# Performance work log

Hardware: AMD Instinct MI355X
Metric: run time of the kernel (lower is better)

The kernel has to match this reference:

```python
import jax, jax.numpy as jnp
import numpy as np

VOCAB, EMBED, UNITS, T, B = 50000, 300, 512, 128, 512


def setup_inputs() -> dict:
    key = jax.random.key(0)
    k1, k2, k3, k4 = jax.random.split(key, 4)
    input_sequence = jax.random.randint(k1, (B, T), 0, VOCAB, dtype=jnp.int32)
    state_h = jnp.zeros((B, UNITS), jnp.float32)
    state_c = jnp.zeros((B, UNITS), jnp.float32)
    # learned params (Keras LSTMCell gate order: i, f, g(cell), o)
    emb_table = jax.random.normal(k2, (VOCAB, EMBED), jnp.float32) * 0.05
    kernel = jax.random.normal(k3, (EMBED, 4 * UNITS), jnp.float32) * 0.05
    rec_kernel = jax.random.normal(k4, (UNITS, 4 * UNITS), jnp.float32) * 0.05
    bias = jnp.zeros((4 * UNITS,), jnp.float32)
    return {"input_sequence": input_sequence, "state_h": state_h, "state_c": state_c,
            "emb_table": emb_table, "kernel": kernel, "rec_kernel": rec_kernel, "bias": bias}


def reference(input_sequence, state_h, state_c, emb_table, kernel, rec_kernel, bias):
    # Embedding with mask_zero=True: token id 0 is masked (state carried through).
    x = emb_table[input_sequence]            # [B, T, E]
    mask = (input_sequence != 0)             # [B, T]
    x_t = jnp.transpose(x, (1, 0, 2))        # [T, B, E]
    m_t = jnp.transpose(mask, (1, 0))        # [T, B]

    def step(carry, inp):
        h, c = carry
        xt, mt = inp
        z = xt @ kernel + h @ rec_kernel + bias          # [B, 4U]
        i, f, g, o = jnp.split(z, 4, axis=-1)
        i = jax.nn.sigmoid(i)
        f = jax.nn.sigmoid(f)
        o = jax.nn.sigmoid(o)
        c_new = f * c + i * jnp.tanh(g)
        h_new = o * jnp.tanh(c_new)
        m = mt[:, None]
        h_new = jnp.where(m, h_new, h)
        c_new = jnp.where(m, c_new, c)
        return (h_new, c_new), h_new

    (h_fin, c_fin), outs = jax.lax.scan(step, (state_h, state_c), (x_t, m_t))
    enc_output = jnp.transpose(outs, (1, 0, 2))          # [B, T, U]
    return enc_output, h_fin, c_fin
```

## Files before the change

kernel.cpp:

```cpp
#include <hip/hip_runtime.h>

#define BATCH 512
#define SEQ   128
#define EMBED 300
#define UNITS 512

typedef short  short8   __attribute__((ext_vector_type(8)));
typedef float  floatx16 __attribute__((ext_vector_type(16)));

#define KXF  19
#define KHF  32

#define SH_B1  0
#define SH_B2  32768
#define SMEM_BYTES (32768 + 38912)

#define WS_FLAGS 0
#define WS_HBUF  4096
#define WS_XBUF  (4096 + 1048576)
#define WS_NEED  (WS_XBUF + 2 * 8 * 38912)

__device__ __forceinline__ unsigned short f2bf(float f) {
  union { float f; unsigned u; } v; v.f = f;
  unsigned r = v.u + 0x7fff + ((v.u >> 16) & 1);
  return (unsigned short)(r >> 16);
}
__device__ __forceinline__ float sigm(float x) { return 1.f / (1.f + __expf(-x)); }
__device__ __forceinline__ float tanh_f(float x) {
  float e = __expf(2.f * x);
  return 1.f - 2.f / (e + 1.f);
}

__device__ __forceinline__ void g_store32(unsigned* p, unsigned v) {
  __hip_atomic_store(p, v, __ATOMIC_RELAXED, __HIP_MEMORY_SCOPE_AGENT);
}
__device__ __forceinline__ unsigned long long g_load64(const void* p) {
  return __hip_atomic_load((const unsigned long long*)p, __ATOMIC_RELAXED,
                           __HIP_MEMORY_SCOPE_AGENT);
}
__device__ __forceinline__ short8 ld_frag(const char* p) {
  union { unsigned long long q[2]; short8 s; } u;
  u.q[0] = g_load64(p);
  u.q[1] = g_load64(p + 8);
  return u.s;
}

__device__ __forceinline__ void poll_ge(const unsigned* gf, int lane, unsigned tgt) {
  const unsigned* p = gf + (lane & 31) * 4;
  for (;;) {
    unsigned v = __hip_atomic_load(p, __ATOMIC_RELAXED, __HIP_MEMORY_SCOPE_AGENT);
    if (__ballot(v >= tgt) == ~0ull) break;
    __builtin_amdgcn_s_sleep(1);
  }
}

#define LDH_GRP(arr, base)                                         \
  do { _Pragma("unroll")                                           \
    for (int j = 0; j < 8; ++j) arr[j] = ld_frag(hrow + ((base) + j) * 32); \
  } while (0)

#define MFMA_H_GRP(arr, base)                                                     \
  do { _Pragma("unroll")                                                          \
    for (int j = 0; j < 8; ++j) {                                                 \
      const int kf = (base) + j;                                                  \
      acc0 = __builtin_amdgcn_mfma_f32_32x32x16_bf16(arr[j], b0[kf], acc0, 0,0,0);\
      short8 p1 = *(const short8*)(sh_b1 + (kf * 64 + lane) * 16);                \
      acc1 = __builtin_amdgcn_mfma_f32_32x32x16_bf16(arr[j], p1, acc1, 0,0,0);    \
    }                                                                             \
  } while (0)

extern "C" __global__ void __launch_bounds__(128, 1)
lstm_enc(const int* __restrict__ seq, const float* __restrict__ h0,
         const float* __restrict__ c0, const float* __restrict__ emb,
         const float* __restrict__ kern, const float* __restrict__ rkern,
         const float* __restrict__ bias, float* __restrict__ out,
         char* __restrict__ ws)
{
  extern __shared__ __align__(16) char smem[];
  char* sh_b1 = smem + SH_B1;
  char* sh_b2 = smem + SH_B2;

  const int tid  = threadIdx.x;
  const int lane = tid & 63;
  const int w    = tid >> 6;
  const int rb   = blockIdx.x & 7;
  const int ug   = blockIdx.x >> 3;

  unsigned* gflags = (unsigned*)(ws + WS_FLAGS) + rb * 128;
  unsigned* myflag = gflags + ug * 4;
  char* hb_[2] = { ws + WS_HBUF, ws + WS_HBUF + 524288 };
  char* xb_[2] = { ws + WS_XBUF + (0 * 8 + rb) * 38912,
                   ws + WS_XBUF + (1 * 8 + rb) * 38912 };

  const int  n    = lane & 31;
  const int  half = lane >> 5;
  const int  u    = ug * 16 + (n & 15);
  const bool lo   = (n < 16);

  const int gcol0 = (lo ? 0    : 512 ) + (n & 15) + ug * 16;
  const int gcol1 = (lo ? 1024 : 1536) + (n & 15) + ug * 16;

  short8 b0[KHF];
#pragma unroll
  for (int kf = 0; kf < KHF; ++kf) {
    int k0 = kf * 16 + half * 8;
    short8 p0, p1;
#pragma unroll
    for (int j = 0; j < 8; ++j) {
      p0[j] = (short)f2bf(rkern[(k0 + j) * 2048 + gcol0]);
      p1[j] = (short)f2bf(rkern[(k0 + j) * 2048 + gcol1]);
    }
    b0[kf] = p0;
    *(short8*)(sh_b1 + (kf * 64 + lane) * 16) = p1;
  }
#pragma unroll
  for (int kf = 0; kf < KXF; ++kf) {
    int k0 = kf * 16 + half * 8;
    short8 p0, p1;
#pragma unroll
    for (int j = 0; j < 8; ++j) {
      int k = k0 + j;
      p0[j] = (short)((k < EMBED) ? f2bf(kern[k * 2048 + gcol0]) : 0);
      p1[j] = (short)((k < EMBED) ? f2bf(kern[k * 2048 + gcol1]) : 0);
    }
    *(short8*)(sh_b2 + ((0 * KXF + kf) * 64 + lane) * 16) = p0;
    *(short8*)(sh_b2 + ((1 * KXF + kf) * 64 + lane) * 16) = p1;
  }

  const float bsi = bias[u], bsf = bias[512 + u], bsg = bias[1024 + u], bso = bias[1536 + u];

  float hreg[16], creg[16];
#pragma unroll
  for (int r = 0; r < 16; ++r) {
    int rowl = (r & 3) + 8 * (r >> 2) + 4 * half;
    int brow = rb * 64 + w * 32 + rowl;
    float hv = h0[brow * 512 + u];
    float cv = c0[brow * 512 + u];
    hreg[r] = hv; creg[r] = cv;
    float hp = __shfl_xor(hv, 1, 64);
    if (lo && !(n & 1)) {
      unsigned d = (unsigned)f2bf(hv) | ((unsigned)f2bf(hp) << 16);
      g_store32((unsigned*)(hb_[1] + brow * 1024 + u * 2), d);
    }
  }

  {
    int r0 = rb * 64 + 2 * ug;
#pragma unroll
    for (int r = 0; r < 2; ++r) {
      int tok = seq[(r0 + r) * SEQ + 0];
      const float* erow = emb + tok * EMBED;
      char* xd = xb_[0] + (2 * ug + r) * 608;
      for (int k2 = tid; k2 < 152; k2 += 128) {
        int k = 2 * k2;
        float e0 = (k     < EMBED) ? erow[k]     : 0.f;
        float e1 = (k + 1 < EMBED) ? erow[k + 1] : 0.f;
        unsigned d = (unsigned)f2bf(e0) | ((unsigned)f2bf(e1) << 16);
        g_store32((unsigned*)(xd + k2 * 4), d);
      }
    }
  }

  __syncthreads();
  if (tid == 0) g_store32(myflag, 1u);
  poll_ge(gflags, lane, 1u);

#pragma unroll 1
  for (int t = 0; t < SEQ; ++t) {
    const char* hsrc = hb_[(t + 1) & 1];
    char*       hdst = hb_[t & 1];
    const char* xsrc = xb_[t & 1];
    char*       xdst = xb_[(t + 1) & 1];

    int tok16[16];
#pragma unroll
    for (int r = 0; r < 16; ++r) {
      int rowl = (r & 3) + 8 * (r >> 2) + 4 * half;
      tok16[r] = seq[(rb * 64 + w * 32 + rowl) * SEQ + t];
    }

    const char* xrow = xsrc + (w * 32 + n) * 608 + half * 16;
    const char* hrow = hsrc + (rb * 64 + w * 32 + n) * 1024 + half * 16;
    short8 xf[KXF];
#pragma unroll
    for (int kf = 0; kf < KXF; ++kf) xf[kf] = ld_frag(xrow + kf * 32);
    short8 hA[8], hB[8];
    LDH_GRP(hA, 0);
    LDH_GRP(hB, 8);

    floatx16 acc0, acc1;
#pragma unroll
    for (int i = 0; i < 16; ++i) { acc0[i] = 0.f; acc1[i] = 0.f; }

#pragma unroll
    for (int kf = 0; kf < KXF; ++kf) {
      short8 p0 = *(const short8*)(sh_b2 + ((0 * KXF + kf) * 64 + lane) * 16);
      short8 p1 = *(const short8*)(sh_b2 + ((1 * KXF + kf) * 64 + lane) * 16);
      acc0 = __builtin_amdgcn_mfma_f32_32x32x16_bf16(xf[kf], p0, acc0, 0, 0, 0);
      acc1 = __builtin_amdgcn_mfma_f32_32x32x16_bf16(xf[kf], p1, acc1, 0, 0, 0);
    }
    MFMA_H_GRP(hA, 0);  LDH_GRP(hA, 16);
    MFMA_H_GRP(hB, 8);  LDH_GRP(hB, 24);
    MFMA_H_GRP(hA, 16);
    MFMA_H_GRP(hB, 24);

#pragma unroll
    for (int r = 0; r < 16; ++r) {
      float a0 = acc0[r], a1 = acc1[r];
      float s0 = __shfl_xor(a0, 16, 64);
      float s1 = __shfl_xor(a1, 16, 64);
      float zi = (lo ? a0 : s0) + bsi;
      float zf = (lo ? s0 : a0) + bsf;
      float zg = (lo ? a1 : s1) + bsg;
      float zo = (lo ? s1 : a1) + bso;
      float iv = sigm(zi), fv = sigm(zf), gv = tanh_f(zg), ov = sigm(zo);
      float cn = fv * creg[r] + iv * gv;
      float hn = ov * tanh_f(cn);
      int rowl = (r & 3) + 8 * (r >> 2) + 4 * half;
      int brow = rb * 64 + w * 32 + rowl;
      if (tok16[r] == 0) { cn = creg[r]; hn = hreg[r]; }
      creg[r] = cn; hreg[r] = hn;
      float hp = __shfl_xor(hn, 1, 64);
      if (lo) {
        out[brow * (SEQ * 512) + t * 512 + u] = hn;
        if (!(n & 1)) {
          unsigned d = (unsigned)f2bf(hn) | ((unsigned)f2bf(hp) << 16);
          g_store32((unsigned*)(hdst + brow * 1024 + u * 2), d);
        }
        if (t == SEQ - 1) {
          out[BATCH * SEQ * 512 + brow * 512 + u] = hn;
          out[BATCH * SEQ * 512 + BATCH * 512 + brow * 512 + u] = cn;
        }
      }
    }

    if (t < SEQ - 1) {
      int r0 = rb * 64 + 2 * ug;
#pragma unroll
      for (int r = 0; r < 2; ++r) {
        int tok = seq[(r0 + r) * SEQ + (t + 1)];
        const float* erow = emb + tok * EMBED;
        char* xd = xdst + (2 * ug + r) * 608;
        for (int k2 = tid; k2 < 152; k2 += 128) {
          int k = 2 * k2;
          float e0 = (k     < EMBED) ? erow[k]     : 0.f;
          float e1 = (k + 1 < EMBED) ? erow[k + 1] : 0.f;
          unsigned d = (unsigned)f2bf(e0) | ((unsigned)f2bf(e1) << 16);
          g_store32((unsigned*)(xd + k2 * 4), d);
        }
      }
      __syncthreads();
      if (tid == 0) g_store32(myflag, (unsigned)(t + 2));
      poll_ge(gflags, lane, (unsigned)(t + 2));
    }
  }
}

extern "C" void kernel_launch(void* const* d_in, const int* in_sizes, int n_in,
                              void* d_out, int out_size, void* d_ws, size_t ws_size,
                              hipStream_t stream) {
  if (ws_size < (size_t)WS_NEED) return;
  const int*   seq   = (const int*)d_in[0];
  const float* h0    = (const float*)d_in[1];
  const float* c0    = (const float*)d_in[2];
  const float* emb   = (const float*)d_in[3];
  const float* kern  = (const float*)d_in[4];
  const float* rkern = (const float*)d_in[5];
  const float* bias  = (const float*)d_in[6];
  float* out = (float*)d_out;

  hipFuncSetAttribute((const void*)lstm_enc,
                      hipFuncAttributeMaxDynamicSharedMemorySize, SMEM_BYTES);
  hipMemsetAsync(d_ws, 0, 4096, stream);
  lstm_enc<<<dim3(256), dim3(128), SMEM_BYTES, stream>>>(
      seq, h0, c0, emb, kern, rkern, bias, out, (char*)d_ws);
}
```

Measured before the change: 2.692 ms.

## Gather embeddings per-lane, overlap x-projection with barrier wait, pad flags

After: 3.046 ms. +13.1%, slower.

```diff
diff --git a/kernel.cpp b/kernel.cpp
--- a/kernel.cpp
+++ b/kernel.cpp
@@ -16,9 +16,8 @@
 #define SMEM_BYTES (32768 + 38912)
 
 #define WS_FLAGS 0
-#define WS_HBUF  4096
-#define WS_XBUF  (4096 + 1048576)
-#define WS_NEED  (WS_XBUF + 2 * 8 * 38912)
+#define WS_HBUF  65536
+#define WS_NEED  (65536 + 2 * 524288)
 
 __device__ __forceinline__ unsigned short f2bf(float f) {
   union { float f; unsigned u; } v; v.f = f;
@@ -46,16 +45,18 @@
 }
 
 __device__ __forceinline__ void poll_ge(const unsigned* gf, int lane, unsigned tgt) {
-  const unsigned* p = gf + (lane & 31) * 4;
+  const unsigned* p = gf + (lane & 31) * 64;
   for (;;) {
-    unsigned v = __hip_atomic_load(p, __ATOMIC_RELAXED, __HIP_MEMORY_SCOPE_AGENT);
+    unsigned v = tgt;
+    if (lane < 32)
+      v = __hip_atomic_load(p, __ATOMIC_RELAXED, __HIP_MEMORY_SCOPE_AGENT);
     if (__ballot(v >= tgt) == ~0ull) break;
     __builtin_amdgcn_s_sleep(1);
   }
 }
 
-#define LDH_GRP(arr, base)                                         \
-  do { _Pragma("unroll")                                           \
+#define LDH_GRP(arr, base)                                                  \
+  do { _Pragma("unroll")                                                    \
     for (int j = 0; j < 8; ++j) arr[j] = ld_frag(hrow + ((base) + j) * 32); \
   } while (0)
 
@@ -86,11 +87,9 @@
   const int rb   = blockIdx.x & 7;
   const int ug   = blockIdx.x >> 3;
 
-  unsigned* gflags = (unsigned*)(ws + WS_FLAGS) + rb * 128;
-  unsigned* myflag = gflags + ug * 4;
+  unsigned* gflags = (unsigned*)(ws + WS_FLAGS) + rb * 2048;
+  unsigned* myflag = gflags + ug * 64;
   char* hb_[2] = { ws + WS_HBUF, ws + WS_HBUF + 524288 };
-  char* xb_[2] = { ws + WS_XBUF + (0 * 8 + rb) * 38912,
-                   ws + WS_XBUF + (1 * 8 + rb) * 38912 };
 
   const int  n    = lane & 31;
   const int  half = lane >> 5;
@@ -144,33 +143,15 @@
     }
   }
 
-  {
-    int r0 = rb * 64 + 2 * ug;
-#pragma unroll
-    for (int r = 0; r < 2; ++r) {
-      int tok = seq[(r0 + r) * SEQ + 0];
-      const float* erow = emb + tok * EMBED;
-      char* xd = xb_[0] + (2 * ug + r) * 608;
-      for (int k2 = tid; k2 < 152; k2 += 128) {
-        int k = 2 * k2;
-        float e0 = (k     < EMBED) ? erow[k]     : 0.f;
-        float e1 = (k + 1 < EMBED) ? erow[k + 1] : 0.f;
-        unsigned d = (unsigned)f2bf(e0) | ((unsigned)f2bf(e1) << 16);
-        g_store32((unsigned*)(xd + k2 * 4), d);
-      }
-    }
-  }
-
   __syncthreads();
   if (tid == 0) g_store32(myflag, 1u);
-  poll_ge(gflags, lane, 1u);
+
+  const int myrow = rb * 64 + w * 32 + n;
 
 #pragma unroll 1
   for (int t = 0; t < SEQ; ++t) {
     const char* hsrc = hb_[(t + 1) & 1];
     char*       hdst = hb_[t & 1];
-    const char* xsrc = xb_[t & 1];
-    char*       xdst = xb_[(t + 1) & 1];
 
     int tok16[16];
 #pragma unroll
@@ -179,26 +160,51 @@
       tok16[r] = seq[(rb * 64 + w * 32 + rowl) * SEQ + t];
     }
 
-    const char* xrow = xsrc + (w * 32 + n) * 608 + half * 16;
+    floatx16 acc0, acc1;
+#pragma unroll
+    for (int i = 0; i < 16; ++i) { acc0[i] = 0.f; acc1[i] = 0.f; }
+
+    {
+      int tok = seq[myrow * SEQ + t];
+      const float* erow = emb + tok * EMBED;
+#pragma unroll
+      for (int kf = 0; kf < KXF; ++kf) {
+        short8 xf;
+        if (kf < 18) {
+          float4 e0 = *(const float4*)(erow + kf * 16 + half * 8);
+          float4 e1 = *(const float4*)(erow + kf * 16 + half * 8 + 4);
+          xf[0] = (short)f2bf(e0.x); xf[1] = (short)f2bf(e0.y);
+          xf[2] = (short)f2bf(e0.z); xf[3] = (short)f2bf(e0.w);
+          xf[4] = (short)f2bf(e1.x); xf[5] = (short)f2bf(e1.y);
+          xf[6] = (short)f2bf(e1.z); xf[7] = (short)f2bf(e1.w);
+        } else {
+          if (half == 0) {
+            float4 e0 = *(const float4*)(erow + 288);
+            float4 e1 = *(const float4*)(erow + 292);
+            xf[0] = (short)f2bf(e0.x); xf[1] = (short)f2bf(e0.y);
+            xf[2] = (short)f2bf(e0.z); xf[3] = (short)f2bf(e0.w);
+            xf[4] = (short)f2bf(e1.x); xf[5] = (short)f2bf(e1.y);
+            xf[6] = (short)f2bf(e1.z); xf[7] = (short)f2bf(e1.w);
+          } else {
+            float4 e0 = *(const float4*)(erow + 296);
+            xf[0] = (short)f2bf(e0.x); xf[1] = (short)f2bf(e0.y);
+            xf[2] = (short)f2bf(e0.z); xf[3] = (short)f2bf(e0.w);
+            xf[4] = 0; xf[5] = 0; xf[6] = 0; xf[7] = 0;
+          }
+        }
+        short8 p0 = *(const short8*)(sh_b2 + ((0 * KXF + kf) * 64 + lane) * 16);
+        short8 p1 = *(const short8*)(sh_b2 + ((1 * KXF + kf) * 64 + lane) * 16);
+        acc0 = __builtin_amdgcn_mfma_f32_32x32x16_bf16(xf, p0, acc0, 0, 0, 0);
+        acc1 = __builtin_amdgcn_mfma_f32_32x32x16_bf16(xf, p1, acc1, 0, 0, 0);
+      }
+    }
+
+    poll_ge(gflags, lane, (unsigned)(t + 1));
+
     const char* hrow = hsrc + (rb * 64 + w * 32 + n) * 1024 + half * 16;
-    short8 xf[KXF];
-#pragma unroll
-    for (int kf = 0; kf < KXF; ++kf) xf[kf] = ld_frag(xrow + kf * 32);
     short8 hA[8], hB[8];
     LDH_GRP(hA, 0);
     LDH_GRP(hB, 8);
-
-    floatx16 acc0, acc1;
-#pragma unroll
-    for (int i = 0; i < 16; ++i) { acc0[i] = 0.f; acc1[i] = 0.f; }
-
-#pragma unroll
-    for (int kf = 0; kf < KXF; ++kf) {
-      short8 p0 = *(const short8*)(sh_b2 + ((0 * KXF + kf) * 64 + lane) * 16);
-      short8 p1 = *(const short8*)(sh_b2 + ((1 * KXF + kf) * 64 + lane) * 16);
-      acc0 = __builtin_amdgcn_mfma_f32_32x32x16_bf16(xf[kf], p0, acc0, 0, 0, 0);
-      acc1 = __builtin_amdgcn_mfma_f32_32x32x16_bf16(xf[kf], p1, acc1, 0, 0, 0);
-    }
     MFMA_H_GRP(hA, 0);  LDH_GRP(hA, 16);
     MFMA_H_GRP(hB, 8);  LDH_GRP(hB, 24);
     MFMA_H_GRP(hA, 16);
@@ -216,42 +222,31 @@
       float iv = sigm(zi), fv = sigm(zf), gv = tanh_f(zg), ov = sigm(zo);
       float cn = fv * creg[r] + iv * gv;
       float hn = ov * tanh_f(cn);
-      int rowl = (r & 3) + 8 * (r >> 2) + 4 * half;
-      int brow = rb * 64 + w * 32 + rowl;
       if (tok16[r] == 0) { cn = creg[r]; hn = hreg[r]; }
       creg[r] = cn; hreg[r] = hn;
       float hp = __shfl_xor(hn, 1, 64);
-      if (lo) {
-        out[brow * (SEQ * 512) + t * 512 + u] = hn;
-        if (!(n & 1)) {
-          unsigned d = (unsigned)f2bf(hn) | ((unsigned)f2bf(hp) << 16);
-          g_store32((unsigned*)(hdst + brow * 1024 + u * 2), d);
-        }
+      if (lo && !(n & 1)) {
+        int rowl = (r & 3) + 8 * (r >> 2) + 4 * half;
+        int brow = rb * 64 + w * 32 + rowl;
+        unsigned d = (unsigned)f2bf(hn) | ((unsigned)f2bf(hp) << 16);
+        g_store32((unsigned*)(hdst + brow * 1024 + u * 2), d);
+      }
+    }
+
+    __syncthreads();
+    if (t < SEQ - 1 && tid == 0) g_store32(myflag, (unsigned)(t + 2));
+
+    if (lo) {
+#pragma unroll
+      for (int r = 0; r < 16; ++r) {
+        int rowl = (r & 3) + 8 * (r >> 2) + 4 * half;
+        int brow = rb * 64 + w * 32 + rowl;
+        out[brow * (SEQ * 512) + t * 512 + u] = hreg[r];
         if (t == SEQ - 1) {
-          out[BATCH * SEQ * 512 + brow * 512 + u] = hn;
-          out[BATCH * SEQ * 512 + BATCH * 512 + brow * 512 + u] = cn;
+          out[BATCH * SEQ * 512 + brow * 512 + u] = hreg[r];
+          out[BATCH * SEQ * 512 + BATCH * 512 + brow * 512 + u] = creg[r];
         }
       }
-    }
-
-    if (t < SEQ - 1) {
-      int r0 = rb * 64 + 2 * ug;
-#pragma unroll
-      for (int r = 0; r < 2; ++r) {
-        int tok = seq[(r0 + r) * SEQ + (t + 1)];
-        const float* erow = emb + tok * EMBED;
-        char* xd = xdst + (2 * ug + r) * 608;
-        for (int k2 = tid; k2 < 152; k2 += 128) {
-          int k = 2 * k2;
-          float e0 = (k     < EMBED) ? erow[k]     : 0.f;
-          float e1 = (k + 1 < EMBED) ? erow[k + 1] : 0.f;
-          unsigned d = (unsigned)f2bf(e0) | ((unsigned)f2bf(e1) << 16);
-          g_store32((unsigned*)(xd + k2 * 4), d);
-        }
-      }
-      __syncthreads();
-      if (tid == 0) g_store32(myflag, (unsigned)(t + 2));
-      poll_ge(gflags, lane, (unsigned)(t + 2));
     }
   }
 }
@@ -271,7 +266,7 @@
 
   hipFuncSetAttribute((const void*)lstm_enc,
                       hipFuncAttributeMaxDynamicSharedMemorySize, SMEM_BYTES);
-  hipMemsetAsync(d_ws, 0, 4096, stream);
+  hipMemsetAsync(d_ws, 0, 65536, stream);
   lstm_enc<<<dim3(256), dim3(128), SMEM_BYTES, stream>>>(
       seq, h0, c0, emb, kern, rkern, bias, out, (char*)d_ws);
 }
```
